# Kernel optimization log

Hardware: AMD Instinct MI355X
Metric: run time of the kernel (lower is better)

Reference implementation:

```python
import jax, jax.numpy as jnp
import numpy as np

POS_HALF = 4   # positive window: [t-4, t+4)
NEG_LEN = 12   # negatives: up to 12 frames on each side of the positive window
K_MAX = 2 * POS_HALF + 2 * NEG_LEN  # 32 candidates max per timestep


def _build_windows(T):
    """Static [T,K_MAX] gather indices + positive/valid masks (numpy, trace-time)."""
    idx = np.zeros((T, K_MAX), np.int32)
    pos_mask = np.zeros((T, K_MAX), bool)
    valid = np.zeros((T, K_MAX), bool)
    for t in range(T):
        start, end = max(0, t - POS_HALF), min(T, t + POS_HALF)
        pos = list(range(start, end))
        neg = list(range(max(0, start - NEG_LEN), start)) + \
              list(range(end, min(T, end + NEG_LEN)))
        comb = pos + neg
        idx[t, :len(comb)] = comb
        valid[t, :len(comb)] = True
        pos_mask[t, :len(pos)] = True
    return jnp.asarray(idx), jnp.asarray(pos_mask), jnp.asarray(valid)


def _directional(q, kv, idx, pos_mask, valid, scale, bias):
    # q, kv: [B,T,D] (L2-normalized); idx/pos_mask/valid: [T,K]
    w = kv[:, idx]  # [B,T,K,D] windowed gather
    logits = jnp.einsum('btd,btkd->btk', q, w) * scale + bias  # [B,T,K]
    sign = jnp.where(pos_mask, 1.0, -1.0)
    loglik = jax.nn.log_sigmoid(sign * logits)
    # per-t: sum over window, mean over batch; then sum over t
    loss = -jnp.where(valid, loglik, 0.0).sum(axis=2).mean(axis=0).sum()
    am = jnp.argmax(jnp.where(valid, logits, -jnp.inf), axis=2)  # [B,T]
    T = q.shape[1]
    correct = pos_mask[jnp.arange(T)[None, :], am].astype(jnp.float32).sum()
    return loss, correct


def setup_inputs() -> dict:
    key = jax.random.key(0)
    k1, k2 = jax.random.split(key)
    B, T, D = 8, 1024, 512
    return {
        "motion_feature": jax.random.normal(k1, (B, T, D), jnp.float32),
        "audio_feature": jax.random.normal(k2, (B, T, D), jnp.float32),
        "logit_scale": jnp.asarray(np.log(1.0 / 0.07), jnp.float32),  # param (pre-exp)
        "logit_bias": jnp.asarray(0.0, jnp.float32),                  # param
    }


def reference(motion_feature, audio_feature, logit_scale, logit_bias):
    B, T, _ = motion_feature.shape
    eps = 1e-12
    m = motion_feature / jnp.clip(
        jnp.linalg.norm(motion_feature, axis=2, keepdims=True), eps)
    a = audio_feature / jnp.clip(
        jnp.linalg.norm(audio_feature, axis=2, keepdims=True), eps)
    scale = jnp.exp(logit_scale)
    idx, pos_mask, valid = _build_windows(T)
    m2a_loss, m2a_correct = _directional(m, a, idx, pos_mask, valid, scale, logit_bias)
    a2m_loss, a2m_correct = _directional(a, m, idx, pos_mask, valid, scale, logit_bias)
    final_loss = (m2a_loss + a2m_loss) / (2 * T)
    total_correct = (m2a_correct + a2m_correct) / (2 * T * B)
    return final_loss, total_correct
```

## Files before the change

kernel.cpp:

```cpp
#include <hip/hip_runtime.h>
#include <hip/hip_bf16.h>
#include <math.h>

#define B_DIM 8
#define T_DIM 1024
#define D_DIM 512
#define BT (B_DIM * T_DIM)
#define NBLK 512

typedef __bf16 bf16x8 __attribute__((ext_vector_type(8)));
typedef float floatx4 __attribute__((ext_vector_type(4)));

__device__ __forceinline__ float wave_reduce_sum(float v) {
#pragma unroll
    for (int off = 32; off > 0; off >>= 1) v += __shfl_xor(v, off, 64);
    return v;
}

__device__ __forceinline__ float softplus(float y) {
    return fmaxf(y, 0.0f) + log1pf(expf(-fabsf(y)));
}

__device__ __forceinline__ bf16x8 cvt8(float4 x, float4 y) {
    union { ushort u[8]; bf16x8 v; } r;
    __hip_bfloat162 h0 = __float22bfloat162_rn(make_float2(x.x, x.y));
    __hip_bfloat162 h1 = __float22bfloat162_rn(make_float2(x.z, x.w));
    __hip_bfloat162 h2 = __float22bfloat162_rn(make_float2(y.x, y.y));
    __hip_bfloat162 h3 = __float22bfloat162_rn(make_float2(y.z, y.w));
    ushort2 p0 = *(ushort2*)&h0, p1 = *(ushort2*)&h1;
    ushort2 p2 = *(ushort2*)&h2, p3 = *(ushort2*)&h3;
    r.u[0] = p0.x; r.u[1] = p0.y; r.u[2] = p1.x; r.u[3] = p1.y;
    r.u[4] = p2.x; r.u[5] = p2.y; r.u[6] = p3.x; r.u[7] = p3.y;
    return r.v;
}

__global__ __launch_bounds__(256, 2) void bigband_kernel(
    const float* __restrict__ m, const float* __restrict__ a,
    const float* __restrict__ pscale, const float* __restrict__ pbias,
    float* __restrict__ part_loss, float* __restrict__ part_corr)
{
    __shared__ float red[4][9][272];
    __shared__ float Sbuf[48][49];
    __shared__ float red2[4][6][16];
    __shared__ float norms[6][16];
    __shared__ float rowpos[16], colpos[16], shl[4];

    int blk = blockIdx.x;
    int b   = blk >> 6;
    int t0  = (blk & 63) << 4;
    int tid  = threadIdx.x;
    int w    = tid >> 6;
    int lane = tid & 63;
    int mrow = lane & 15;
    int kgrp = lane >> 4;
    int koff = w * 128 + kgrp * 8;

    const float* mb = m + ((size_t)b << 19);
    const float* ab = a + ((size_t)b << 19);

    const float* mp[3]; const float* ap[3];
#pragma unroll
    for (int s = 0; s < 3; ++s) {
        int r = t0 - 16 + s * 16 + mrow;
        r = min(max(r, 0), T_DIM - 1);
        mp[s] = mb + (size_t)r * D_DIM + koff;
        ap[s] = ab + (size_t)r * D_DIM + koff;
    }

    floatx4 acc[3][3];
#pragma unroll
    for (int ti = 0; ti < 3; ++ti)
#pragma unroll
        for (int tj = 0; tj < 3; ++tj) acc[ti][tj] = (floatx4){0.f,0.f,0.f,0.f};
    float ssm[3] = {0.f,0.f,0.f}, ssa[3] = {0.f,0.f,0.f};

#pragma unroll
    for (int ks = 0; ks < 4; ++ks) {
        bf16x8 am[3], av[3];
#pragma unroll
        for (int s = 0; s < 3; ++s) {
            float4 x = *(const float4*)(mp[s] + ks * 32);
            float4 y = *(const float4*)(mp[s] + ks * 32 + 4);
            ssm[s] += x.x*x.x + x.y*x.y + x.z*x.z + x.w*x.w
                    + y.x*y.x + y.y*y.y + y.z*y.z + y.w*y.w;
            am[s] = cvt8(x, y);
            float4 u = *(const float4*)(ap[s] + ks * 32);
            float4 v = *(const float4*)(ap[s] + ks * 32 + 4);
            ssa[s] += u.x*u.x + u.y*u.y + u.z*u.z + u.w*u.w
                    + v.x*v.x + v.y*v.y + v.z*v.z + v.w*v.w;
            av[s] = cvt8(u, v);
        }
#pragma unroll
        for (int ti = 0; ti < 3; ++ti)
#pragma unroll
            for (int tj = 0; tj < 3; ++tj)
                acc[ti][tj] = __builtin_amdgcn_mfma_f32_16x16x32_bf16(
                    am[ti], av[tj], acc[ti][tj], 0, 0, 0);
    }

#pragma unroll
    for (int off = 16; off <= 32; off <<= 1) {
#pragma unroll
        for (int s = 0; s < 3; ++s) {
            ssm[s] += __shfl_xor(ssm[s], off, 64);
            ssa[s] += __shfl_xor(ssa[s], off, 64);
        }
    }
    if (kgrp == 0) {
#pragma unroll
        for (int s = 0; s < 3; ++s) {
            red2[w][s][mrow]     = ssm[s];
            red2[w][3 + s][mrow] = ssa[s];
        }
    }
#pragma unroll
    for (int ti = 0; ti < 3; ++ti)
#pragma unroll
        for (int tj = 0; tj < 3; ++tj)
#pragma unroll
            for (int r = 0; r < 4; ++r)
                red[w][ti * 3 + tj][(kgrp * 4 + r) * 17 + mrow] = acc[ti][tj][r];
    __syncthreads();

    if (tid < 96) {
        int slot = tid >> 4, mr = tid & 15;
        float ss = red2[0][slot][mr] + red2[1][slot][mr]
                 + red2[2][slot][mr] + red2[3][slot][mr];
        norms[slot][mr] = 1.0f / fmaxf(sqrtf(ss), 1e-12f);
    }
    int rho = tid >> 4, kap = tid & 15;
#pragma unroll
    for (int ti = 0; ti < 3; ++ti)
#pragma unroll
        for (int tj = 0; tj < 3; ++tj) {
            int tt = ti * 3 + tj;
            float s4 = red[0][tt][rho * 17 + kap] + red[1][tt][rho * 17 + kap]
                     + red[2][tt][rho * 17 + kap] + red[3][tt][rho * 17 + kap];
            Sbuf[ti * 16 + rho][tj * 16 + kap] = s4;
        }
    __syncthreads();

    float scale = expf(pscale[0]), bias = pbias[0];
    int i = rho, cc = kap;
    float loss = 0.0f;

    {
        float im_u = norms[1][i];
        float mmax = -1e30f, mpos = 0.0f;
#pragma unroll
        for (int tj = 0; tj < 3; ++tj) {
            int v  = tj * 16 + cc;
            int dd = v - i;
            int c  = t0 - 16 + v;
            if (dd >= 0 && dd < 32 && c >= 0 && c < T_DIM) {
                float sv = Sbuf[16 + i][v] * norms[3 + tj][cc];
                float logit = sv * im_u * scale + bias;
                bool pos = (dd >= 12) && (dd <= 19);
                loss += softplus(pos ? -logit : logit);
                if (sv > mmax) { mmax = sv; mpos = pos ? 1.0f : 0.0f; }
            }
        }
#pragma unroll
        for (int off = 1; off < 16; off <<= 1) {
            float ov = __shfl_xor(mmax, off, 64);
            float op = __shfl_xor(mpos, off, 64);
            if (ov > mmax) { mmax = ov; mpos = op; }
        }
        if (cc == 0) rowpos[i] = mpos;
    }

    {
        float ia_v = norms[4][i];
        float amax = -1e30f, apos = 0.0f;
#pragma unroll
        for (int tj = 0; tj < 3; ++tj) {
            int u2 = tj * 16 + cc;
            int ee = u2 - i;
            int r  = t0 - 16 + u2;
            if (ee >= 0 && ee < 32 && r >= 0 && r < T_DIM) {
                float sv = Sbuf[u2][16 + i] * norms[tj][cc];
                float logit = sv * ia_v * scale + bias;
                bool pos = (ee >= 12) && (ee <= 19);
                loss += softplus(pos ? -logit : logit);
                if (sv > amax) { amax = sv; apos = pos ? 1.0f : 0.0f; }
            }
        }
#pragma unroll
        for (int off = 1; off < 16; off <<= 1) {
            float ov = __shfl_xor(amax, off, 64);
            float op = __shfl_xor(apos, off, 64);
            if (ov > amax) { amax = ov; apos = op; }
        }
        if (cc == 0) colpos[i] = apos;
    }

    loss = wave_reduce_sum(loss);
    if (lane == 0) shl[w] = loss;
    __syncthreads();
    if (tid == 0) {
        float C = 0.0f;
#pragma unroll
        for (int r = 0; r < 16; ++r) C += rowpos[r] + colpos[r];
        part_loss[blk] = shl[0] + shl[1] + shl[2] + shl[3];
        part_corr[blk] = C;
    }
}

__global__ __launch_bounds__(256) void finalsum_kernel(
    const float* __restrict__ part_loss, const float* __restrict__ part_corr,
    float* __restrict__ out)
{
    int tid = threadIdx.x;
    float l = part_loss[tid] + part_loss[tid + 256];
    float c = part_corr[tid] + part_corr[tid + 256];
    l = wave_reduce_sum(l);
    c = wave_reduce_sum(c);
    __shared__ float shl[4], shc[4];
    int w = tid >> 6, lane = tid & 63;
    if (lane == 0) { shl[w] = l; shc[w] = c; }
    __syncthreads();
    if (tid == 0) {
        out[0] = (shl[0] + shl[1] + shl[2] + shl[3]) / 16384.0f;
        out[1] = (shc[0] + shc[1] + shc[2] + shc[3]) / 16384.0f;
    }
}

extern "C" void kernel_launch(void* const* d_in, const int* in_sizes, int n_in,
                              void* d_out, int out_size, void* d_ws, size_t ws_size,
                              hipStream_t stream)
{
    const float* m  = (const float*)d_in[0];
    const float* a  = (const float*)d_in[1];
    const float* ps = (const float*)d_in[2];
    const float* pb = (const float*)d_in[3];
    float* out = (float*)d_out;

    float* part_loss = (float*)d_ws;
    float* part_corr = part_loss + NBLK;

    bigband_kernel<<<NBLK, 256, 0, stream>>>(m, a, ps, pb, part_loss, part_corr);
    finalsum_kernel<<<1, 256, 0, stream>>>(part_loss, part_corr, out);
}
```

Before: 93.05 us.

## Compute only the five needed similarity tiles and split K across eight waves

The kernel now computes only the five 16x16 similarity tiles actually read by the loss (the centre row and column of the 3x3 tile grid) instead of all nine, cutting MFMA work and the LDS reduction traffic. The block grows to 512 threads with eight waves each covering 64 of the feature dimension, which halves per-wave load and accumulator work and raises parallelism. The two loss directions now run on separate halves of the block instead of serially. The cost is a cross-wave reduction over eight partials instead of four and higher per-block LDS use, which may limit occupancy.

```diff
diff --git a/kernel.cpp b/kernel.cpp
--- a/kernel.cpp
+++ b/kernel.cpp
@@ -34,16 +34,16 @@
     return r.v;
 }
 
-__global__ __launch_bounds__(256, 2) void bigband_kernel(
+__global__ __launch_bounds__(512, 4) void crossband_kernel(
     const float* __restrict__ m, const float* __restrict__ a,
     const float* __restrict__ pscale, const float* __restrict__ pbias,
     float* __restrict__ part_loss, float* __restrict__ part_corr)
 {
-    __shared__ float red[4][9][272];
+    __shared__ float red[8][5][272];
     __shared__ float Sbuf[48][49];
-    __shared__ float red2[4][6][16];
+    __shared__ float red2[8][6][16];
     __shared__ float norms[6][16];
-    __shared__ float rowpos[16], colpos[16], shl[4];
+    __shared__ float rowpos[16], colpos[16], shl[8];
 
     int blk = blockIdx.x;
     int b   = blk >> 6;
@@ -53,7 +53,7 @@
     int lane = tid & 63;
     int mrow = lane & 15;
     int kgrp = lane >> 4;
-    int koff = w * 128 + kgrp * 8;
+    int koff = w * 64 + kgrp * 8;
 
     const float* mb = m + ((size_t)b << 19);
     const float* ab = a + ((size_t)b << 19);
@@ -67,15 +67,13 @@
         ap[s] = ab + (size_t)r * D_DIM + koff;
     }
 
-    floatx4 acc[3][3];
-#pragma unroll
-    for (int ti = 0; ti < 3; ++ti)
-#pragma unroll
-        for (int tj = 0; tj < 3; ++tj) acc[ti][tj] = (floatx4){0.f,0.f,0.f,0.f};
+    floatx4 acc[5];
+#pragma unroll
+    for (int q = 0; q < 5; ++q) acc[q] = (floatx4){0.f,0.f,0.f,0.f};
     float ssm[3] = {0.f,0.f,0.f}, ssa[3] = {0.f,0.f,0.f};
 
 #pragma unroll
-    for (int ks = 0; ks < 4; ++ks) {
+    for (int ks = 0; ks < 2; ++ks) {
         bf16x8 am[3], av[3];
 #pragma unroll
         for (int s = 0; s < 3; ++s) {
@@ -90,12 +88,11 @@
                     + v.x*v.x + v.y*v.y + v.z*v.z + v.w*v.w;
             av[s] = cvt8(u, v);
         }
-#pragma unroll
-        for (int ti = 0; ti < 3; ++ti)
-#pragma unroll
-            for (int tj = 0; tj < 3; ++tj)
-                acc[ti][tj] = __builtin_amdgcn_mfma_f32_16x16x32_bf16(
-                    am[ti], av[tj], acc[ti][tj], 0, 0, 0);
+        acc[0] = __builtin_amdgcn_mfma_f32_16x16x32_bf16(am[1], av[0], acc[0], 0, 0, 0);
+        acc[1] = __builtin_amdgcn_mfma_f32_16x16x32_bf16(am[1], av[1], acc[1], 0, 0, 0);
+        acc[2] = __builtin_amdgcn_mfma_f32_16x16x32_bf16(am[1], av[2], acc[2], 0, 0, 0);
+        acc[3] = __builtin_amdgcn_mfma_f32_16x16x32_bf16(am[0], av[1], acc[3], 0, 0, 0);
+        acc[4] = __builtin_amdgcn_mfma_f32_16x16x32_bf16(am[2], av[1], acc[4], 0, 0, 0);
     }
 
 #pragma unroll
@@ -114,37 +111,43 @@
         }
     }
 #pragma unroll
-    for (int ti = 0; ti < 3; ++ti)
-#pragma unroll
-        for (int tj = 0; tj < 3; ++tj)
-#pragma unroll
-            for (int r = 0; r < 4; ++r)
-                red[w][ti * 3 + tj][(kgrp * 4 + r) * 17 + mrow] = acc[ti][tj][r];
+    for (int q = 0; q < 5; ++q)
+#pragma unroll
+        for (int r = 0; r < 4; ++r)
+            red[w][q][(kgrp * 4 + r) * 17 + mrow] = acc[q][r];
     __syncthreads();
 
     if (tid < 96) {
         int slot = tid >> 4, mr = tid & 15;
-        float ss = red2[0][slot][mr] + red2[1][slot][mr]
-                 + red2[2][slot][mr] + red2[3][slot][mr];
+        float ss = 0.f;
+#pragma unroll
+        for (int ww = 0; ww < 8; ++ww) ss += red2[ww][slot][mr];
         norms[slot][mr] = 1.0f / fmaxf(sqrtf(ss), 1e-12f);
     }
-    int rho = tid >> 4, kap = tid & 15;
-#pragma unroll
-    for (int ti = 0; ti < 3; ++ti)
-#pragma unroll
-        for (int tj = 0; tj < 3; ++tj) {
-            int tt = ti * 3 + tj;
-            float s4 = red[0][tt][rho * 17 + kap] + red[1][tt][rho * 17 + kap]
-                     + red[2][tt][rho * 17 + kap] + red[3][tt][rho * 17 + kap];
-            Sbuf[ti * 16 + rho][tj * 16 + kap] = s4;
-        }
+    {
+        const int tu[5] = {16, 16, 16, 0, 32};
+        const int tv[5] = {0, 16, 32, 16, 16};
+#pragma unroll
+        for (int e = 0; e < 3; ++e) {
+            int idx = tid + e * 512;
+            if (idx < 1280) {
+                int q = idx >> 8, r2 = idx & 255;
+                int rho = r2 >> 4, kap = r2 & 15;
+                float s4 = 0.f;
+#pragma unroll
+                for (int ww = 0; ww < 8; ++ww)
+                    s4 += red[ww][q][rho * 17 + kap];
+                Sbuf[tu[q] + rho][tv[q] + kap] = s4;
+            }
+        }
+    }
     __syncthreads();
 
     float scale = expf(pscale[0]), bias = pbias[0];
-    int i = rho, cc = kap;
     float loss = 0.0f;
 
-    {
+    if (tid < 256) {
+        int i = tid >> 4, cc = tid & 15;
         float im_u = norms[1][i];
         float mmax = -1e30f, mpos = 0.0f;
 #pragma unroll
@@ -167,9 +170,9 @@
             if (ov > mmax) { mmax = ov; mpos = op; }
         }
         if (cc == 0) rowpos[i] = mpos;
-    }
-
-    {
+    } else {
+        int t2 = tid - 256;
+        int i = t2 >> 4, cc = t2 & 15;
         float ia_v = norms[4][i];
         float amax = -1e30f, apos = 0.0f;
 #pragma unroll
@@ -198,10 +201,12 @@
     if (lane == 0) shl[w] = loss;
     __syncthreads();
     if (tid == 0) {
-        float C = 0.0f;
+        float L = 0.0f, C = 0.0f;
+#pragma unroll
+        for (int r = 0; r < 8; ++r) L += shl[r];
 #pragma unroll
         for (int r = 0; r < 16; ++r) C += rowpos[r] + colpos[r];
-        part_loss[blk] = shl[0] + shl[1] + shl[2] + shl[3];
+        part_loss[blk] = L;
         part_corr[blk] = C;
     }
 }
@@ -238,6 +243,6 @@
     float* part_loss = (float*)d_ws;
     float* part_corr = part_loss + NBLK;
 
-    bigband_kernel<<<NBLK, 256, 0, stream>>>(m, a, ps, pb, part_loss, part_corr);
+    crossband_kernel<<<NBLK, 512, 0, stream>>>(m, a, ps, pb, part_loss, part_corr);
     finalsum_kernel<<<1, 256, 0, stream>>>(part_loss, part_corr, out);
 }
```

Result: faster. 90.72 us (-2.5%).
